# Optimization experiments

Measured on AMD Instinct MI355X. Metric: run time of the kernel, lower is better.

## Reference

```python
import jax, jax.numpy as jnp
import numpy as np

MARGIN = 2.0
N_STREAM = 4
BRANCH_WEIGHT = np.ones(N_STREAM, dtype=np.float32)  # default branch_weight = [1.0]*n_stream
ALPHA = 1.0 / N_STREAM  # MultistreamLoss default alpha
BETA = 1.0              # MultistreamLoss default beta
EPS = 1e-4


def _ranking(preds, labels):
    # sum over pairs i<j of relu(-(p[j]-p[i]) * sign(l[j]-l[i]) + margin)
    n = preds.shape[0]
    d = preds[None, :] - preds[:, None]          # d[i, j] = p[j] - p[i]
    s = jnp.sign(labels[None, :] - labels[:, None])
    h = jax.nn.relu(-d * s + MARGIN)             # [n, n]
    mask = jnp.triu(jnp.ones((n, n), dtype=bool), k=1)  # j > i
    return jnp.sum(jnp.where(mask, h, jnp.zeros((), h.dtype)))


def setup_inputs() -> dict:
    key = jax.random.key(0)
    k1, k2, k3 = jax.random.split(key, 3)
    n = 4096
    scores = jax.random.normal(k1, (N_STREAM, n), dtype=jnp.float32)
    pred = jax.random.normal(k2, (n,), dtype=jnp.float32)
    label = jax.random.normal(k3, (n,), dtype=jnp.float32)
    return {"scores": scores, "pred": pred, "label": label}


def reference(scores, pred, label):
    # branch ranking losses, one per stream
    branch = jax.vmap(lambda s: _ranking(s, label))(scores)       # [N_STREAM]
    branch_loss = jnp.sum(jnp.asarray(BRANCH_WEIGHT) * branch)

    # BatchRankingMSE_Loss (alpha=None -> 1.0, beta=None -> grad-norm ratio, no renorm)
    mse = jnp.mean((pred - label) ** 2)
    rank = _ranking(pred, label)
    g1 = jnp.linalg.norm(jax.grad(lambda p: jnp.mean((p - label) ** 2))(pred))
    g2 = jnp.linalg.norm(jax.grad(lambda p: _ranking(p, label))(pred))
    beta_w = jax.lax.stop_gradient(g1 / (g2 + EPS))  # computed under no_grad in torch
    pred_loss = 1.0 * mse + beta_w * rank

    return ALPHA * branch_loss + BETA * pred_loss
```

## Files before the change

### kernel.cpp

```cpp
#include <hip/hip_runtime.h>
#include <math.h>

#define N 4096
#define MARGINF 2.0f
#define EPSF 1e-4f

constexpr int TILE = 256;
constexpr int NT = N / TILE;
constexpr int NDIAGTILES = NT * (NT + 1) / 2;
constexpr int NSCORE_BLK = 4 * NDIAGTILES;
constexpr int NPRED_BLK = NT * NT;
constexpr int NBLK = NSCORE_BLK + NPRED_BLK;
constexpr int GRAD_OFF = 1024;


__global__ __launch_bounds__(256) void pair_kernel(
    const float* __restrict__ scores, const float* __restrict__ pred,
    const float* __restrict__ label, float* __restrict__ ws)
{
    __shared__ float red[4];

    const int bid = blockIdx.x;
    const int tid = threadIdx.x;
    float sum0 = 0.f, sum1 = 0.f;

    if (bid < NSCORE_BLK) {
        const int stream = bid / NDIAGTILES;
        int t = bid % NDIAGTILES;
        int ti = 0;
        while (t >= NT - ti) { t -= NT - ti; ++ti; }
        const int tj = ti + t;
        const float* __restrict__ p = scores + stream * N;

        const int r = ti * TILE + tid;
        const int c0 = tj * TILE;
        const float rk = p[r];
        const float lk = label[r];

        if (ti != tj) {
            #pragma unroll 4
            for (int j = 0; j < TILE; j += 4) {
                const float4 l4 = *(const float4*)&label[c0 + j];
                const float4 p4 = *(const float4*)&p[c0 + j];
                auto body = [&](float lm, float pm, float& acc) {
                    const unsigned sgn = __float_as_uint(lm - lk) & 0x80000000u;
                    const float x = __uint_as_float(__float_as_uint(pm - rk) ^ sgn);
                    acc += fmaxf(MARGINF - x, 0.f);
                };
                body(l4.x, p4.x, sum0); body(l4.y, p4.y, sum1);
                body(l4.z, p4.z, sum0); body(l4.w, p4.w, sum1);
            }
        } else {
            #pragma unroll 4
            for (int j = 0; j < TILE; j += 4) {
                const float4 l4 = *(const float4*)&label[c0 + j];
                const float4 p4 = *(const float4*)&p[c0 + j];
                auto body = [&](float lm, float pm, int cc, float& acc) {
                    const unsigned sgn = __float_as_uint(lm - lk) & 0x80000000u;
                    const float x = __uint_as_float(__float_as_uint(pm - rk) ^ sgn);
                    const float h = fmaxf(MARGINF - x, 0.f);
                    acc += (cc > tid) ? h : 0.f;
                };
                body(l4.x, p4.x, j + 0, sum0); body(l4.y, p4.y, j + 1, sum1);
                body(l4.z, p4.z, j + 2, sum0); body(l4.w, p4.w, j + 3, sum1);
            }
        }
    } else {
        const int rem = bid - NSCORE_BLK;
        const int rowblk = rem >> 4;
        const int ch = rem & (NT - 1);
        const int r = rowblk * TILE + tid;
        const int c0 = ch * TILE;
        const float rk = pred[r];
        const float lk = label[r];

        float grad0 = 0.f, grad1 = 0.f;
        #pragma unroll 4
        for (int j = 0; j < TILE; j += 4) {
            const float4 l4 = *(const float4*)&label[c0 + j];
            const float4 p4 = *(const float4*)&pred[c0 + j];
            auto body = [&](float lm, float pm, float& acc, float& gacc) {
                const unsigned sgn = __float_as_uint(lm - lk) & 0x80000000u;
                const float x = __uint_as_float(__float_as_uint(pm - rk) ^ sgn);
                const float z = MARGINF - x;
                acc += fmaxf(z, 0.f);
                const float sf = __uint_as_float(0x3f800000u ^ sgn);
                gacc += (z > 0.f) ? sf : 0.f;
            };
            body(l4.x, p4.x, sum0, grad0); body(l4.y, p4.y, sum1, grad1);
            body(l4.z, p4.z, sum0, grad0); body(l4.w, p4.w, sum1, grad1);
        }
        float grad = grad0 + grad1;
        if (rowblk == ch) grad -= 1.0f;
        ws[GRAD_OFF + r * 16 + ch] = grad;
    }

    float sum = sum0 + sum1;
    #pragma unroll
    for (int off = 32; off > 0; off >>= 1)
        sum += __shfl_xor(sum, off, 64);
    const int wid = tid >> 6;
    const int lane = tid & 63;
    if (lane == 0) red[wid] = sum;
    __syncthreads();
    if (tid == 0)
        ws[bid] = red[0] + red[1] + red[2] + red[3];
}

__global__ __launch_bounds__(256) void finalize_kernel(
    const float* __restrict__ pred, const float* __restrict__ label,
    const float* __restrict__ ws, float* __restrict__ out)
{
    __shared__ float lds[16];
    const int tid = threadIdx.x;

    float sse = 0.f, g2sq = 0.f;
    #pragma unroll
    for (int k = 0; k < NT; ++k) {
        const int i = k * 256 + tid;
        const float d = pred[i] - label[i];
        sse += d * d;
        const float4* gp = (const float4*)(ws + GRAD_OFF + i * 16);
        const float4 a = gp[0], b = gp[1], c = gp[2], e = gp[3];
        const float g = (a.x + a.y + a.z + a.w) + (b.x + b.y + b.z + b.w)
                      + (c.x + c.y + c.z + c.w) + (e.x + e.y + e.z + e.w);
        g2sq += g * g;
    }

    float br = ws[tid] + ws[tid + 256] + ((tid < 32) ? ws[512 + tid] : 0.f);
    float pr = ws[NSCORE_BLK + tid];

    #pragma unroll
    for (int off = 32; off > 0; off >>= 1) {
        sse  += __shfl_xor(sse,  off, 64);
        g2sq += __shfl_xor(g2sq, off, 64);
        br   += __shfl_xor(br,   off, 64);
        pr   += __shfl_xor(pr,   off, 64);
    }
    const int wid = tid >> 6;
    const int lane = tid & 63;
    if (lane == 0) {
        lds[wid] = sse; lds[4 + wid] = g2sq;
        lds[8 + wid] = br; lds[12 + wid] = pr;
    }
    __syncthreads();
    if (tid == 0) {
        const float sseT  = lds[0] + lds[1] + lds[2] + lds[3];
        const float g2sqT = lds[4] + lds[5] + lds[6] + lds[7];
        const float brT   = lds[8] + lds[9] + lds[10] + lds[11];
        const float prT   = lds[12] + lds[13] + lds[14] + lds[15];
        const float rankp = (prT - (float)N * MARGINF) * 0.5f;
        const float mse = sseT / (float)N;
        const float g1 = (2.0f / (float)N) * sqrtf(sseT);
        const float g2 = sqrtf(g2sqT);
        const float beta = g1 / (g2 + EPSF);
        out[0] = 0.25f * brT + mse + beta * rankp;
    }
}

extern "C" void kernel_launch(void* const* d_in, const int* in_sizes, int n_in,
                              void* d_out, int out_size, void* d_ws, size_t ws_size,
                              hipStream_t stream) {
    const float* scores = (const float*)d_in[0];
    const float* pred   = (const float*)d_in[1];
    const float* label  = (const float*)d_in[2];
    float* ws  = (float*)d_ws;
    float* out = (float*)d_out;

    pair_kernel<<<NBLK, 256, 0, stream>>>(scores, pred, label, ws);
    finalize_kernel<<<1, 256, 0, stream>>>(pred, label, ws, out);
}
```

Measured before the change: 24.81 us.

## Compute pairwise hinge terms in packed fp16 with LDS-staged column chunks

Moves the pairwise hinge computation from fp32 to packed half2 arithmetic and accumulates with the fdot2 instruction. Column labels and scores are converted once per block into LDS. Tiles are split into 128-column chunks, which doubles the block count, and the gradient partial layout widens to 32 entries per row. The aim is to halve the VALU work per pair, at the cost of fp16 rounding (round-toward-zero conversion) in differences and hinge values, which may break accuracy tolerance.

```diff
diff --git a/kernel.cpp b/kernel.cpp
--- a/kernel.cpp
+++ b/kernel.cpp
@@ -5,94 +5,156 @@
 #define MARGINF 2.0f
 #define EPSF 1e-4f
 
+typedef __fp16   half2v __attribute__((ext_vector_type(2)));
+typedef _Float16 f16x2  __attribute__((ext_vector_type(2)));
+
+__device__ __forceinline__ unsigned h2u(half2v h){ return __builtin_bit_cast(unsigned, h); }
+__device__ __forceinline__ half2v  u2h(unsigned u){ return __builtin_bit_cast(half2v, u); }
+
+__device__ __forceinline__ float dot2acc(half2v a, half2v b, float c){
+#if __has_builtin(__builtin_amdgcn_fdot2)
+    return __builtin_amdgcn_fdot2(__builtin_bit_cast(f16x2, a),
+                                  __builtin_bit_cast(f16x2, b), c, false);
+#else
+    return c + (float)a.x * (float)b.x + (float)a.y * (float)b.y;
+#endif
+}
+
 constexpr int TILE = 256;
 constexpr int NT = N / TILE;
 constexpr int NDIAGTILES = NT * (NT + 1) / 2;
-constexpr int NSCORE_BLK = 4 * NDIAGTILES;
-constexpr int NPRED_BLK = NT * NT;
+constexpr int CHUNK = 128;
+constexpr int NSCORE_BLK = 4 * NDIAGTILES * 2;
+constexpr int NPRED_BLK = NT * (N / CHUNK);
 constexpr int NBLK = NSCORE_BLK + NPRED_BLK;
-constexpr int GRAD_OFF = 1024;
+constexpr int GRAD_OFF = 2048;
 
 
 __global__ __launch_bounds__(256) void pair_kernel(
     const float* __restrict__ scores, const float* __restrict__ pred,
     const float* __restrict__ label, float* __restrict__ ws)
 {
+    __shared__ unsigned lab16[CHUNK / 2];
+    __shared__ unsigned col16[CHUNK / 2];
     __shared__ float red[4];
 
     const int bid = blockIdx.x;
     const int tid = threadIdx.x;
+
+    const half2v zero2 = {(__fp16)0.0f, (__fp16)0.0f};
+    const half2v one2  = {(__fp16)1.0f, (__fp16)1.0f};
+    const half2v two2  = {(__fp16)2.0f, (__fp16)2.0f};
+    const half2v big2  = {(__fp16)65504.0f, (__fp16)65504.0f};
+
     float sum0 = 0.f, sum1 = 0.f;
 
     if (bid < NSCORE_BLK) {
-        const int stream = bid / NDIAGTILES;
-        int t = bid % NDIAGTILES;
+        const int stream = bid / (NDIAGTILES * 2);
+        const int t = bid % (NDIAGTILES * 2);
+        int tIdx = t >> 1;
+        const int h = t & 1;
         int ti = 0;
-        while (t >= NT - ti) { t -= NT - ti; ++ti; }
-        const int tj = ti + t;
+        while (tIdx >= NT - ti) { tIdx -= NT - ti; ++ti; }
+        const int tj = ti + tIdx;
         const float* __restrict__ p = scores + stream * N;
-
+        const int c0 = tj * TILE + h * CHUNK;
+
+        if (tid < CHUNK / 2) {
+            const float2 lf = *(const float2*)&label[c0 + 2 * tid];
+            lab16[tid] = h2u(__builtin_amdgcn_cvt_pkrtz(lf.x, lf.y));
+        } else if (tid < CHUNK) {
+            const int q = tid - CHUNK / 2;
+            const float2 pf = *(const float2*)&p[c0 + 2 * q];
+            col16[q] = h2u(__builtin_amdgcn_cvt_pkrtz(pf.x, pf.y));
+        }
         const int r = ti * TILE + tid;
-        const int c0 = tj * TILE;
-        const float rk = p[r];
-        const float lk = label[r];
+        const float rkf = p[r];
+        const float lkf = label[r];
+        const half2v rk2 = __builtin_amdgcn_cvt_pkrtz(rkf, rkf);
+        const half2v lk2 = __builtin_amdgcn_cvt_pkrtz(lkf, lkf);
+        __syncthreads();
 
         if (ti != tj) {
+            auto body2 = [&](unsigned lm2u, unsigned pm2u, float& acc) {
+                const half2v ld2 = u2h(lm2u) - lk2;
+                const unsigned sgn = h2u(ld2) & 0x80008000u;
+                const half2v pd2 = u2h(pm2u) - rk2;
+                const half2v x2 = u2h(h2u(pd2) ^ sgn);
+                const half2v m2 = __builtin_elementwise_max(two2 - x2, zero2);
+                acc = dot2acc(m2, one2, acc);
+            };
             #pragma unroll 4
-            for (int j = 0; j < TILE; j += 4) {
-                const float4 l4 = *(const float4*)&label[c0 + j];
-                const float4 p4 = *(const float4*)&p[c0 + j];
-                auto body = [&](float lm, float pm, float& acc) {
-                    const unsigned sgn = __float_as_uint(lm - lk) & 0x80000000u;
-                    const float x = __uint_as_float(__float_as_uint(pm - rk) ^ sgn);
-                    acc += fmaxf(MARGINF - x, 0.f);
-                };
-                body(l4.x, p4.x, sum0); body(l4.y, p4.y, sum1);
-                body(l4.z, p4.z, sum0); body(l4.w, p4.w, sum1);
+            for (int q4 = 0; q4 < CHUNK / 8; ++q4) {
+                const uint4 l4 = *(const uint4*)&lab16[q4 * 4];
+                const uint4 s4 = *(const uint4*)&col16[q4 * 4];
+                body2(l4.x, s4.x, sum0); body2(l4.y, s4.y, sum1);
+                body2(l4.z, s4.z, sum0); body2(l4.w, s4.w, sum1);
             }
         } else {
+            const int cbase = h * CHUNK;
+            auto body2m = [&](unsigned lm2u, unsigned pm2u, int cc0, float& acc) {
+                const half2v ld2 = u2h(lm2u) - lk2;
+                const unsigned sgn = h2u(ld2) & 0x80008000u;
+                const half2v pd2 = u2h(pm2u) - rk2;
+                const half2v x2 = u2h(h2u(pd2) ^ sgn);
+                const half2v m2 = __builtin_elementwise_max(two2 - x2, zero2);
+                const unsigned mu = (cc0 + 1 > tid) ? ((cc0 > tid) ? 0x3C003C00u
+                                                                   : 0x3C000000u)
+                                                    : 0u;
+                acc = dot2acc(m2, u2h(mu), acc);
+            };
             #pragma unroll 4
-            for (int j = 0; j < TILE; j += 4) {
-                const float4 l4 = *(const float4*)&label[c0 + j];
-                const float4 p4 = *(const float4*)&p[c0 + j];
-                auto body = [&](float lm, float pm, int cc, float& acc) {
-                    const unsigned sgn = __float_as_uint(lm - lk) & 0x80000000u;
-                    const float x = __uint_as_float(__float_as_uint(pm - rk) ^ sgn);
-                    const float h = fmaxf(MARGINF - x, 0.f);
-                    acc += (cc > tid) ? h : 0.f;
-                };
-                body(l4.x, p4.x, j + 0, sum0); body(l4.y, p4.y, j + 1, sum1);
-                body(l4.z, p4.z, j + 2, sum0); body(l4.w, p4.w, j + 3, sum1);
+            for (int q4 = 0; q4 < CHUNK / 8; ++q4) {
+                const uint4 l4 = *(const uint4*)&lab16[q4 * 4];
+                const uint4 s4 = *(const uint4*)&col16[q4 * 4];
+                const int cc = cbase + q4 * 8;
+                body2m(l4.x, s4.x, cc + 0, sum0); body2m(l4.y, s4.y, cc + 2, sum1);
+                body2m(l4.z, s4.z, cc + 4, sum0); body2m(l4.w, s4.w, cc + 6, sum1);
             }
         }
     } else {
         const int rem = bid - NSCORE_BLK;
-        const int rowblk = rem >> 4;
-        const int ch = rem & (NT - 1);
+        const int rowblk = rem >> 5;
+        const int ch = rem & 31;
+        const int c0 = ch * CHUNK;
+
+        if (tid < CHUNK / 2) {
+            const float2 lf = *(const float2*)&label[c0 + 2 * tid];
+            lab16[tid] = h2u(__builtin_amdgcn_cvt_pkrtz(lf.x, lf.y));
+        } else if (tid < CHUNK) {
+            const int q = tid - CHUNK / 2;
+            const float2 pf = *(const float2*)&pred[c0 + 2 * q];
+            col16[q] = h2u(__builtin_amdgcn_cvt_pkrtz(pf.x, pf.y));
+        }
         const int r = rowblk * TILE + tid;
-        const int c0 = ch * TILE;
-        const float rk = pred[r];
-        const float lk = label[r];
+        const float rkf = pred[r];
+        const float lkf = label[r];
+        const half2v rk2 = __builtin_amdgcn_cvt_pkrtz(rkf, rkf);
+        const half2v lk2 = __builtin_amdgcn_cvt_pkrtz(lkf, lkf);
+        __syncthreads();
 
         float grad0 = 0.f, grad1 = 0.f;
+        auto body2g = [&](unsigned lm2u, unsigned pm2u, float& acc, float& gacc) {
+            const half2v ld2 = u2h(lm2u) - lk2;
+            const unsigned sgn = h2u(ld2) & 0x80008000u;
+            const half2v pd2 = u2h(pm2u) - rk2;
+            const half2v x2 = u2h(h2u(pd2) ^ sgn);
+            const half2v m2 = __builtin_elementwise_max(two2 - x2, zero2);
+            acc = dot2acc(m2, one2, acc);
+            const half2v ind2 = __builtin_elementwise_min(m2 * big2, one2);
+            const unsigned su = h2u(ind2) ^ sgn;
+            gacc = dot2acc(u2h(su), one2, gacc);
+        };
         #pragma unroll 4
-        for (int j = 0; j < TILE; j += 4) {
-            const float4 l4 = *(const float4*)&label[c0 + j];
-            const float4 p4 = *(const float4*)&pred[c0 + j];
-            auto body = [&](float lm, float pm, float& acc, float& gacc) {
-                const unsigned sgn = __float_as_uint(lm - lk) & 0x80000000u;
-                const float x = __uint_as_float(__float_as_uint(pm - rk) ^ sgn);
-                const float z = MARGINF - x;
-                acc += fmaxf(z, 0.f);
-                const float sf = __uint_as_float(0x3f800000u ^ sgn);
-                gacc += (z > 0.f) ? sf : 0.f;
-            };
-            body(l4.x, p4.x, sum0, grad0); body(l4.y, p4.y, sum1, grad1);
-            body(l4.z, p4.z, sum0, grad0); body(l4.w, p4.w, sum1, grad1);
+        for (int q4 = 0; q4 < CHUNK / 8; ++q4) {
+            const uint4 l4 = *(const uint4*)&lab16[q4 * 4];
+            const uint4 s4 = *(const uint4*)&col16[q4 * 4];
+            body2g(l4.x, s4.x, sum0, grad0); body2g(l4.y, s4.y, sum1, grad1);
+            body2g(l4.z, s4.z, sum0, grad0); body2g(l4.w, s4.w, sum1, grad1);
         }
         float grad = grad0 + grad1;
-        if (rowblk == ch) grad -= 1.0f;
-        ws[GRAD_OFF + r * 16 + ch] = grad;
+        if ((r >> 7) == ch) grad -= 1.0f;
+        ws[GRAD_OFF + r * 32 + ch] = grad;
     }
 
     float sum = sum0 + sum1;
@@ -120,15 +182,19 @@
         const int i = k * 256 + tid;
         const float d = pred[i] - label[i];
         sse += d * d;
-        const float4* gp = (const float4*)(ws + GRAD_OFF + i * 16);
-        const float4 a = gp[0], b = gp[1], c = gp[2], e = gp[3];
-        const float g = (a.x + a.y + a.z + a.w) + (b.x + b.y + b.z + b.w)
-                      + (c.x + c.y + c.z + c.w) + (e.x + e.y + e.z + e.w);
+        const float4* gp = (const float4*)(ws + GRAD_OFF + i * 32);
+        float g = 0.f;
+        #pragma unroll
+        for (int q = 0; q < 8; ++q) {
+            const float4 a = gp[q];
+            g += (a.x + a.y) + (a.z + a.w);
+        }
         g2sq += g * g;
     }
 
-    float br = ws[tid] + ws[tid + 256] + ((tid < 32) ? ws[512 + tid] : 0.f);
-    float pr = ws[NSCORE_BLK + tid];
+    float br = ws[tid] + ws[tid + 256] + ws[tid + 512] + ws[tid + 768]
+             + ((tid < 64) ? ws[1024 + tid] : 0.f);
+    float pr = ws[NSCORE_BLK + tid] + ws[NSCORE_BLK + 256 + tid];
 
     #pragma unroll
     for (int off = 32; off > 0; off >>= 1) {
```

After: 37.51 us. 1.51x slower.
